# Kernel tuning notes

Hardware: AMD Instinct MI355X
Metric: run time of the kernel (lower is better)

## Reference

```python
import jax, jax.numpy as jnp
import numpy as np

N_FFT = 2048
HOP = 512
WIN = 2048
PAD = N_FFT // 2  # center padding, n_fft // 2


def setup_inputs() -> dict:
    key = jax.random.key(0)
    x = jax.random.normal(key, (16, 262144), dtype=jnp.float32)
    # periodic Hann window, identical to torch.hann_window(2048)
    window = (0.5 - 0.5 * jnp.cos(2.0 * jnp.pi * jnp.arange(WIN) / WIN)).astype(jnp.float32)
    return {"x": x, "window": window}


def reference(x, window):
    # x: [B, T]; center reflect-pad by n_fft//2 on both sides (matches F.pad mode='reflect')
    xp = jnp.pad(x, ((0, 0), (PAD, PAD)), mode="reflect")
    n_frames = (xp.shape[-1] - N_FFT) // HOP + 1  # static
    # strided framing (replaces the identity-conv im2col in the original)
    idx = jnp.arange(n_frames)[:, None] * HOP + jnp.arange(N_FFT)[None, :]  # [F, n_fft]
    frames = xp[:, idx] * window  # [B, F, n_fft], windowed frames
    # windowed DFT; rfft of windowed frame == F.linear(frames, fft_k) in the original
    spec = jnp.fft.rfft(frames, axis=-1)  # [B, F, n_fft//2+1] complex
    real = jnp.real(spec).transpose(0, 2, 1)  # [B, dim, F]
    imag = jnp.imag(spec).transpose(0, 2, 1)  # [B, dim, F]
    return (real, imag)
```

## Files before the change

kernel.cpp:

```cpp
#include <hip/hip_runtime.h>


#define N_FFT   2048
#define LOG2N   11
#define HOP     512
#define PADL    1024
#define NBINS   1025
#define NFRAMES 513
#define NBATCH  16
#define TLEN    262144

#define HALF_OUT ((size_t)NBATCH * NBINS * NFRAMES)

__device__ __forceinline__ int pidx(int a) { return a + (a >> 5); }

__device__ __forceinline__ int refl(int j) {
    if (j < 0)          j = -j;
    else if (j >= TLEN) j = 2 * TLEN - 2 - j;
    return j;
}

__device__ __forceinline__ float2 cmul(float2 a, float2 w) {
    return make_float2(fmaf(a.x, w.x, -a.y * w.y), fmaf(a.x, w.y, a.y * w.x));
}
__device__ __forceinline__ float2 cadd(float2 a, float2 b) {
    return make_float2(a.x + b.x, a.y + b.y);
}
__device__ __forceinline__ float2 csub(float2 a, float2 b) {
    return make_float2(a.x - b.x, a.y - b.y);
}
__device__ __forceinline__ float2 csqr(float2 w) {
    return make_float2(fmaf(w.x, w.x, -w.y * w.y), 2.0f * w.x * w.y);
}

template <int H, int L2H>
__device__ __forceinline__ void octet_pass(float2* __restrict__ zc, int q) {
    const int p    = q & (H - 1);
    const int base = ((q >> L2H) << (L2H + 3)) + p;
    int ia[8];
#pragma unroll
    for (int m = 0; m < 8; ++m) ia[m] = pidx(base + m * H);
    float2 v0 = zc[ia[0]], v1 = zc[ia[1]], v2 = zc[ia[2]], v3 = zc[ia[3]];
    float2 v4 = zc[ia[4]], v5 = zc[ia[5]], v6 = zc[ia[6]], v7 = zc[ia[7]];

    float2 w1, w2, w3;
    if (H == 1) {
        w3 = make_float2(1.0f, 0.0f); w2 = w3; w1 = w3;
    } else {
        float s, c;
        __sincosf((float)p * (-3.14159265358979323846f / (4.0f * (float)H)), &s, &c);
        w3 = make_float2(c, s);
        w2 = csqr(w3);
        w1 = csqr(w2);
    }

    float2 t;
    t = cmul(v1, w1); v1 = csub(v0, t); v0 = cadd(v0, t);
    t = cmul(v3, w1); v3 = csub(v2, t); v2 = cadd(v2, t);
    t = cmul(v5, w1); v5 = csub(v4, t); v4 = cadd(v4, t);
    t = cmul(v7, w1); v7 = csub(v6, t); v6 = cadd(v6, t);
    const float2 w2m = make_float2(w2.y, -w2.x);
    t = cmul(v2, w2);  v2 = csub(v0, t); v0 = cadd(v0, t);
    t = cmul(v3, w2m); v3 = csub(v1, t); v1 = cadd(v1, t);
    t = cmul(v6, w2);  v6 = csub(v4, t); v4 = cadd(v4, t);
    t = cmul(v7, w2m); v7 = csub(v5, t); v5 = cadd(v5, t);
    const float R = 0.70710678118654752f;
    const float2 w3o  = make_float2((w3.x + w3.y) * R, (w3.y - w3.x) * R);
    const float2 w3m  = make_float2(w3.y, -w3.x);
    const float2 w3mo = make_float2(w3o.y, -w3o.x);
    t = cmul(v4, w3);   v4 = csub(v0, t); v0 = cadd(v0, t);
    t = cmul(v5, w3o);  v5 = csub(v1, t); v1 = cadd(v1, t);
    t = cmul(v6, w3m);  v6 = csub(v2, t); v2 = cadd(v2, t);
    t = cmul(v7, w3mo); v7 = csub(v3, t); v3 = cadd(v3, t);

    zc[ia[0]] = v0; zc[ia[1]] = v1; zc[ia[2]] = v2; zc[ia[3]] = v3;
    zc[ia[4]] = v4; zc[ia[5]] = v5; zc[ia[6]] = v6; zc[ia[7]] = v7;
}

__global__ __launch_bounds__(1024) void stft_one(
    const float* __restrict__ x,
    const float* __restrict__ window,
    float* __restrict__ out)
{
    __shared__ float2 z[9][2112];

    const int d     = blockIdx.x + 32 * blockIdx.y;
    const int pair  = (d >> 4) * 8 + (d & 7);
    const int gg    = 2 * pair + ((d >> 3) & 1);
    const int b     = gg >> 5;
    const int g     = gg & 31;
    const int tid   = threadIdx.x;
    const int f0    = g * 16;
    const int nsub  = (g == 31) ? 9 : 8;

    const float* xb = x + (size_t)b * TLEN;
    for (int idx = tid; idx < nsub * 2048; idx += 1024) {
        const int c  = idx >> 11;
        const int n  = idx & 2047;
        const int fa = f0 + 2 * c;
        const float w  = window[n];
        const float va = xb[refl(fa * HOP - PADL + n)] * w;
        const float vb = xb[refl((fa + 1) * HOP - PADL + n)] * w;
        const int r = (int)(__brev((unsigned)n) >> (32 - LOG2N));
        z[c][pidx(r)] = make_float2(va, vb);
    }
    __syncthreads();

    for (int idx = tid; idx < nsub * 256; idx += 1024)
        octet_pass<1, 0>(z[idx >> 8], idx & 255);
    __syncthreads();
    for (int idx = tid; idx < nsub * 256; idx += 1024)
        octet_pass<8, 3>(z[idx >> 8], idx & 255);
    __syncthreads();
    for (int idx = tid; idx < nsub * 256; idx += 1024)
        octet_pass<64, 6>(z[idx >> 8], idx & 255);
    __syncthreads();

    for (int idx = tid; idx < nsub * 512; idx += 1024) {
        const int c = idx >> 9;
        const int p = idx & 511;
        float s, cc;
        __sincosf((float)p * (-3.14159265358979323846f / 1024.0f), &s, &cc);
        const float2 w2  = make_float2(cc, s);
        const float2 w1  = csqr(w2);
        const float2 w2m = make_float2(w2.y, -w2.x);
        const int i0 = pidx(p), i1 = pidx(p + 512), i2 = pidx(p + 1024), i3 = pidx(p + 1536);
        float2 v0 = z[c][i0], v1 = z[c][i1], v2 = z[c][i2], v3 = z[c][i3];
        float2 t;
        t = cmul(v1, w1); v1 = csub(v0, t); v0 = cadd(v0, t);
        t = cmul(v3, w1); v3 = csub(v2, t); v2 = cadd(v2, t);
        t = cmul(v2, w2);  v2 = csub(v0, t); v0 = cadd(v0, t);
        t = cmul(v3, w2m); v3 = csub(v1, t); v1 = cadd(v1, t);
        z[c][i0] = v0; z[c][i1] = v1; z[c][i2] = v2; z[c][i3] = v3;
    }
    __syncthreads();

    float* __restrict__ outr = out;
    float* __restrict__ outi = out + HALF_OUT;
    for (int k = tid; k < NBINS; k += 1024) {
        const int km = (N_FFT - k) & (N_FFT - 1);
        const size_t orow = ((size_t)b * NBINS + (size_t)k) * NFRAMES + (size_t)f0;
#pragma unroll
        for (int c = 0; c < 8; ++c) {
            const float2 zk = z[c][pidx(k)];
            const float2 zr = z[c][pidx(km)];
            outr[orow + 2 * c]     = 0.5f * (zk.x + zr.x);
            outr[orow + 2 * c + 1] = 0.5f * (zk.y + zr.y);
            outi[orow + 2 * c]     = 0.5f * (zk.y - zr.y);
            outi[orow + 2 * c + 1] = 0.5f * (zr.x - zk.x);
        }
        if (nsub == 9) {
            const float2 zk = z[8][pidx(k)];
            const float2 zr = z[8][pidx(km)];
            outr[orow + 16] = 0.5f * (zk.x + zr.x);
            outi[orow + 16] = 0.5f * (zk.y - zr.y);
        }
    }
}

extern "C" void kernel_launch(void* const* d_in, const int* in_sizes, int n_in,
                              void* d_out, int out_size, void* d_ws, size_t ws_size,
                              hipStream_t stream) {
    const float* x      = (const float*)d_in[0];
    const float* window = (const float*)d_in[1];
    float* out          = (float*)d_out;

    dim3 grid(32, NBATCH);
    stft_one<<<grid, 1024, 0, stream>>>(x, window, out);
}
```

Measured before the change: 127.7 us.

## Split STFT into per-frame-pair FFT kernel plus separate aligned transpose kernel

Replaces the single large-block kernel, which ran 512 blocks of 1024 threads each handling 16 frames, with two kernels. The first kernel computes one frame pair per 256-thread block and writes frame-major complex spectra to workspace. The second kernel transposes tiles into the bin-major real/imag outputs with row writes aligned to 16-element boundaries. The split is meant to raise occupancy and make stores coalesced, in exchange for an extra round trip of the full spectrum through global memory and a second launch. The original kernel is kept as a fallback when the workspace is too small.

```diff
diff --git a/kernel.cpp b/kernel.cpp
--- a/kernel.cpp
+++ b/kernel.cpp
@@ -77,6 +77,111 @@
     zc[ia[4]] = v4; zc[ia[5]] = v5; zc[ia[6]] = v6; zc[ia[7]] = v7;
 }
 
+__global__ __launch_bounds__(256) void stft_fft8(
+    const float* __restrict__ x,
+    const float* __restrict__ window,
+    float2* __restrict__ spec2)
+{
+    __shared__ float2 z[2112];
+
+    const int g   = blockIdx.x;
+    const int b   = blockIdx.y;
+    const int t   = threadIdx.x;
+    const int fa  = 2 * g;
+    const bool hasb = (fa + 1) < NFRAMES;
+
+    const float* xb = x + (size_t)b * TLEN;
+    const int basea = fa * HOP - PADL;
+    const int baseb = (fa + 1) * HOP - PADL;
+#pragma unroll
+    for (int it = 0; it < 8; ++it) {
+        const int n = t + it * 256;
+        const float w  = window[n];
+        const float va = xb[refl(basea + n)] * w;
+        const float vb = xb[refl(baseb + n)] * w;
+        const int r = (int)(__brev((unsigned)n) >> (32 - LOG2N));
+        z[pidx(r)] = make_float2(va, vb);
+    }
+    __syncthreads();
+
+    octet_pass<1, 0>(z, t);   __syncthreads();
+    octet_pass<8, 3>(z, t);   __syncthreads();
+    octet_pass<64, 6>(z, t);  __syncthreads();
+
+#pragma unroll
+    for (int it = 0; it < 2; ++it) {
+        const int p = t + it * 256;
+        float s, cc;
+        __sincosf((float)p * (-3.14159265358979323846f / 1024.0f), &s, &cc);
+        const float2 w2  = make_float2(cc, s);
+        const float2 w1  = csqr(w2);
+        const float2 w2m = make_float2(w2.y, -w2.x);
+        const int i0 = pidx(p), i1 = pidx(p + 512), i2 = pidx(p + 1024), i3 = pidx(p + 1536);
+        float2 v0 = z[i0], v1 = z[i1], v2 = z[i2], v3 = z[i3];
+        float2 tt;
+        tt = cmul(v1, w1); v1 = csub(v0, tt); v0 = cadd(v0, tt);
+        tt = cmul(v3, w1); v3 = csub(v2, tt); v2 = cadd(v2, tt);
+        tt = cmul(v2, w2);  v2 = csub(v0, tt); v0 = cadd(v0, tt);
+        tt = cmul(v3, w2m); v3 = csub(v1, tt); v1 = cadd(v1, tt);
+        z[i0] = v0; z[i1] = v1; z[i2] = v2; z[i3] = v3;
+    }
+    __syncthreads();
+
+    const size_t rowa = ((size_t)b * NFRAMES + fa) * NBINS;
+    const size_t rowb = rowa + NBINS;
+    for (int k = t; k < NBINS; k += 256) {
+        const float2 zk = z[pidx(k)];
+        const float2 zr = z[pidx((N_FFT - k) & (N_FFT - 1))];
+        spec2[rowa + k] = make_float2(0.5f * (zk.x + zr.x), 0.5f * (zk.y - zr.y));
+        if (hasb)
+            spec2[rowb + k] = make_float2(0.5f * (zk.y + zr.y), 0.5f * (zr.x - zk.x));
+    }
+}
+
+__global__ __launch_bounds__(256) void transpose_aligned(
+    const float2* __restrict__ spec2,
+    float* __restrict__ out)
+{
+    __shared__ float2 tile[144][65];
+
+    const int fj = blockIdx.x;
+    const int kt = blockIdx.y;
+    const int b  = blockIdx.z;
+    const int F0 = fj * 128;
+    const int k0 = kt * 64;
+    const int tid = threadIdx.x;
+
+    const float2* sp = spec2 + (size_t)b * NFRAMES * NBINS;
+    for (int i = tid; i < 144 * 64; i += 256) {
+        const int fl  = i >> 6;
+        const int kin = i & 63;
+        const int f = F0 + fl;
+        const int k = k0 + kin;
+        tile[fl][kin] = (f < NFRAMES && k < NBINS) ? sp[(size_t)f * NBINS + k]
+                                                   : make_float2(0.0f, 0.0f);
+    }
+    __syncthreads();
+
+    float* __restrict__ outr = out;
+    float* __restrict__ outi = out + HALF_OUT;
+    for (int i = tid; i < 64 * 144; i += 256) {
+        const int kin = i / 144;
+        const int j   = i - kin * 144;
+        const int k   = k0 + kin;
+        if (k >= NBINS) continue;
+        const size_t rowbase = ((size_t)b * NBINS + k) * NFRAMES;
+        const int a  = (int)((16 - (rowbase & 15)) & 15);
+        const int W0 = (fj == 0) ? 0       : F0 + a;
+        const int W1 = (fj == 3) ? NFRAMES : F0 + 128 + a;
+        const int f  = W0 + j;
+        if (f < W1) {
+            const float2 v = tile[f - F0][kin];
+            outr[rowbase + f] = v.x;
+            outi[rowbase + f] = v.y;
+        }
+    }
+}
+
 __global__ __launch_bounds__(1024) void stft_one(
     const float* __restrict__ x,
     const float* __restrict__ window,
@@ -165,6 +270,15 @@
     const float* window = (const float*)d_in[1];
     float* out          = (float*)d_out;
 
-    dim3 grid(32, NBATCH);
-    stft_one<<<grid, 1024, 0, stream>>>(x, window, out);
-}
+    const size_t need = (size_t)NBATCH * NFRAMES * NBINS * sizeof(float2);
+    if (ws_size >= need) {
+        float2* spec2 = (float2*)d_ws;
+        dim3 ga((NFRAMES + 1) / 2, NBATCH);
+        stft_fft8<<<ga, 256, 0, stream>>>(x, window, spec2);
+        dim3 gb(4, 17, NBATCH);
+        transpose_aligned<<<gb, 256, 0, stream>>>(spec2, out);
+    } else {
+        dim3 grid(32, NBATCH);
+        stft_one<<<grid, 1024, 0, stream>>>(x, window, out);
+    }
+}
```

New measurement: 147.0 us. 15.1% more time.
